# Kernel tuning notes

Measured on AMD Instinct MI355X. Metric: run time of the kernel, lower is better.

## Reference

```python
import jax, jax.numpy as jnp
import numpy as np

M = 8192      # number of simplices (edges)
F_IN = 32
F_OUT = 32
K1 = 3        # lower Laplacian filter order
K2 = 3        # upper Laplacian filter order


def setup_inputs() -> dict:
    key = jax.random.key(0)
    kx, kl, ku, kw = jax.random.split(key, 4)
    x = jax.random.normal(kx, (M, F_IN), dtype=jnp.float32)
    # scale Laplacians so the Chebyshev recursion stays numerically tame
    scale = 1.0 / np.sqrt(M)
    Ll = jax.random.normal(kl, (M, M), dtype=jnp.float32) * scale
    Lu = jax.random.normal(ku, (M, M), dtype=jnp.float32) * scale
    # xavier-uniform-ish init for W (F_in, F_out, 1+K1+K2)
    gain = np.sqrt(2.0)  # relu gain as in reset_parameters
    bound = gain * np.sqrt(6.0 / (F_IN + F_OUT))
    W = jax.random.uniform(kw, (F_IN, F_OUT, 1 + K1 + K2), dtype=jnp.float32,
                           minval=-bound, maxval=bound)
    return {"x": x, "Ll": Ll, "Lu": Lu, "W": W}


def chebyshev(L, K, x):
    """Chebyshev terms T_1..T_K of L applied to x, stacked on a trailing dim.
    T_0 = x, T_1 = L x, T_k = 2 L T_{k-1} - T_{k-2}. Returns [M, F, K]."""
    t_prev = x
    t_cur = L @ x
    terms = [t_cur]
    for _ in range(K - 1):
        t_next = 2.0 * (L @ t_cur) - t_prev
        t_prev, t_cur = t_cur, t_next
        terms.append(t_cur)
    return jnp.stack(terms, axis=2)


def reference(x, Ll, Lu, W):
    # identity term I @ x == x  -> [M, F_in, 1]
    Ix = x[:, :, None]
    Xl = chebyshev(Ll, K1, x)          # [M, F_in, K1]
    Xu = chebyshev(Lu, K2, x)          # [M, F_in, K2]
    X = jnp.concatenate([Ix, Xl, Xu], axis=2)  # [M, F_in, 1+K1+K2]
    # per-order projection; dropout has p=0.0 so it is the identity
    y = jnp.einsum('nik,iok->no', X, W)        # [M, F_out]
    return y
```

## Files before the change

kernel.cpp:

```cpp
#include <hip/hip_runtime.h>
#include <hip/hip_bf16.h>
#include <stdint.h>

#define Mdim 8192
#define KSTEPS 256

typedef __attribute__((ext_vector_type(8))) short short8v;
typedef __attribute__((ext_vector_type(4))) float f32x4;
typedef __attribute__((ext_vector_type(2))) float f32x2;

static __device__ __forceinline__ short bf16c(float f) {
  __hip_bfloat16 h = __float2bfloat16(f);
  union { __hip_bfloat16 h; short s; } c; c.h = h;
  return c.s;
}

__global__ __launch_bounds__(256)
void repack_x(const float* __restrict__ x, short* __restrict__ Bp)
{
  int t = blockIdx.x * 256 + threadIdx.x;
  int l = t & 63, h = (t >> 6) & 1, ks = t >> 7;
  int col = h * 16 + (l & 15);
  int kbase = ks * 32 + ((l >> 4) << 3);
  short8v v;
#pragma unroll
  for (int j = 0; j < 8; ++j) v[j] = bf16c(x[(size_t)(kbase + j) * 32 + col]);
  reinterpret_cast<short8v*>(Bp)[t] = v;
}

__global__ __launch_bounds__(256)
void convert_t1(const float* __restrict__ src, const short* __restrict__ Bx,
                short* __restrict__ dst, float* __restrict__ Pt1)
{
  __shared__ __align__(16) char sh[16 * 1032 * 2];
  short (*Lb)[1032] = reinterpret_cast<short (*)[1032]>(sh);

  const int tile = blockIdx.x >> 3;
  const int slab = blockIdx.x & 7;
  const int t = threadIdx.x;
  const int lane = t & 63;
  const int wid  = t >> 6;

  for (int i = 0; i < 16; ++i) {
    const f32x4* p = reinterpret_cast<const f32x4*>(
        src + ((size_t)tile * 16 + i) * Mdim + slab * 1024) + t;
    f32x4 a = __builtin_nontemporal_load(p);
    short* q = &Lb[i][t * 4];
    q[0] = bf16c(a[0]); q[1] = bf16c(a[1]); q[2] = bf16c(a[2]); q[3] = bf16c(a[3]);
  }
  __syncthreads();

  const short8v* bx8 = reinterpret_cast<const short8v*>(Bx);
  f32x4 acc0 = {0.f, 0.f, 0.f, 0.f};
  f32x4 acc1 = {0.f, 0.f, 0.f, 0.f};
#pragma unroll
  for (int it = 0; it < 8; ++it) {
    const int ksl = it * 4 + wid;
    short8v av = *reinterpret_cast<const short8v*>(
        &Lb[lane & 15][ksl * 32 + ((lane >> 4) << 3)]);
    reinterpret_cast<short8v*>(dst)[(size_t)(tile * 256 + slab * 32 + ksl) * 64 + lane] = av;
    const int gks = slab * 32 + ksl;
    short8v b0 = bx8[(size_t)(gks << 1) * 64 + lane];
    short8v b1 = bx8[(size_t)((gks << 1) + 1) * 64 + lane];
    acc0 = __builtin_amdgcn_mfma_f32_16x16x32_bf16(av, b0, acc0, 0, 0, 0);
    acc1 = __builtin_amdgcn_mfma_f32_16x16x32_bf16(av, b1, acc1, 0, 0, 0);
  }

  __syncthreads();
  float* Clf = reinterpret_cast<float*>(sh);
  {
    const int crow = (lane >> 4) << 2;
    const int ccol = lane & 15;
#pragma unroll
    for (int q = 0; q < 4; ++q) {
      Clf[((wid * 16) + crow + q) * 32 + ccol] = acc0[q];
      Clf[((wid * 16) + crow + q) * 32 + 16 + ccol] = acc1[q];
    }
  }
  __syncthreads();
  {
    const int e = t * 2;
    const int row = e >> 5, col = e & 31;
    float v0 = Clf[row * 32 + col] + Clf[(16 + row) * 32 + col]
             + Clf[(32 + row) * 32 + col] + Clf[(48 + row) * 32 + col];
    float v1 = Clf[row * 32 + col + 1] + Clf[(16 + row) * 32 + col + 1]
             + Clf[(32 + row) * 32 + col + 1] + Clf[(48 + row) * 32 + col + 1];
    f32x2 o; o[0] = v0; o[1] = v1;
    *reinterpret_cast<f32x2*>(Pt1 + (size_t)(tile * 8 + slab) * 512 + e) = o;
  }
}

__global__ __launch_bounds__(256)
void reduce_t1(const float* __restrict__ Pt1, float* __restrict__ Tout,
               short* __restrict__ BpOut)
{
  __shared__ float Cred[16][32];
  const int tile = blockIdx.x;
  const int t = threadIdx.x;
  const int e = t * 2;
  float s0 = 0.f, s1 = 0.f;
#pragma unroll
  for (int s = 0; s < 8; ++s) {
    f32x2 v = *reinterpret_cast<const f32x2*>(Pt1 + (size_t)(tile * 8 + s) * 512 + e);
    s0 += v[0]; s1 += v[1];
  }
  f32x2 o; o[0] = s0; o[1] = s1;
  *reinterpret_cast<f32x2*>(Tout + (size_t)tile * 512 + e) = o;
  Cred[e >> 5][e & 31] = s0;
  Cred[e >> 5][(e & 31) + 1] = s1;
  __syncthreads();
  if (t < 64) {
    const int r0 = tile << 4;
    const int ksOut = r0 >> 5;
    const int sub = (r0 >> 4) & 1;
    const int h = t >> 5;
    const int lp = (t & 31) + sub * 32;
    const int col = h * 16 + (lp & 15);
    const int lrbase = (lp & 16) ? 8 : 0;
    short8v v;
#pragma unroll
    for (int j = 0; j < 8; ++j) v[j] = bf16c(Cred[lrbase + j][col]);
    reinterpret_cast<short8v*>(BpOut)[(ksOut << 1 | h) * 64 + lp] = v;
  }
}

template<int HASPREV>
__global__ __launch_bounds__(512)
void gemm_stage(const short* __restrict__ As, const short* __restrict__ Bps,
                const float* __restrict__ Tprev, float* __restrict__ Tout,
                short* __restrict__ BpOut)
{
  const int bTile = blockIdx.x;
  const int lane = threadIdx.x & 63;
  const int wid  = threadIdx.x >> 6;
  const int r0 = bTile << 4;
  const int ksbase = wid * 32;

  const short8v* aF = reinterpret_cast<const short8v*>(As)
                      + ((size_t)bTile * 256 + ksbase) * 64 + lane;
  const short8v* bF = reinterpret_cast<const short8v*>(Bps)
                      + (size_t)ksbase * 128 + lane;

  f32x4 acc0 = {0.f, 0.f, 0.f, 0.f};
  f32x4 acc1 = {0.f, 0.f, 0.f, 0.f};

#pragma unroll 8
  for (int ks = 0; ks < 32; ++ks) {
    short8v av = aF[ks * 64];
    short8v b0 = bF[ks * 128];
    short8v b1 = bF[ks * 128 + 64];
    acc0 = __builtin_amdgcn_mfma_f32_16x16x32_bf16(av, b0, acc0, 0, 0, 0);
    acc1 = __builtin_amdgcn_mfma_f32_16x16x32_bf16(av, b1, acc1, 0, 0, 0);
  }

  __shared__ float Cl[8][16][32];
  __shared__ float Cred[16][32];
  {
    const int crow = (lane >> 4) << 2;
    const int ccol = lane & 15;
#pragma unroll
    for (int q = 0; q < 4; ++q) {
      Cl[wid][crow + q][ccol] = acc0[q];
      Cl[wid][crow + q][16 + ccol] = acc1[q];
    }
  }
  __syncthreads();
  {
    const int t = threadIdx.x;
    const int row = t >> 5, col = t & 31;
    float v = Cl[0][row][col] + Cl[1][row][col] + Cl[2][row][col] + Cl[3][row][col]
            + Cl[4][row][col] + Cl[5][row][col] + Cl[6][row][col] + Cl[7][row][col];
    if constexpr (HASPREV) {
      v = 2.f * v - Tprev[(size_t)r0 * 32 + t];
    }
    Tout[(size_t)r0 * 32 + t] = v;
    Cred[row][col] = v;
  }
  __syncthreads();
  if (threadIdx.x < 64) {
    const int t = threadIdx.x;
    const int ksOut = r0 >> 5;
    const int sub = (r0 >> 4) & 1;
    const int h = t >> 5;
    const int lp = (t & 31) + sub * 32;
    const int col = h * 16 + (lp & 15);
    const int lrbase = (lp & 16) ? 8 : 0;
    short8v v;
#pragma unroll
    for (int j = 0; j < 8; ++j) v[j] = bf16c(Cred[lrbase + j][col]);
    reinterpret_cast<short8v*>(BpOut)[(ksOut << 1 | h) * 64 + lp] = v;
  }
}

template<int HASPREV>
__global__ __launch_bounds__(512)
void gemm_f32_stage(const float* __restrict__ Af, const short8v* __restrict__ Bp,
                    const float* __restrict__ Tprev, float* __restrict__ Tout,
                    short* __restrict__ BpOut)
{
  const int lane = threadIdx.x & 63;
  const int wid  = threadIdx.x >> 6;
  const int r0 = blockIdx.x << 4;
  const int arow = r0 + (lane & 15);
  const int koff = (lane >> 4) << 3;
  const int ksbase = wid * 32;

  f32x4 acc0 = {0.f, 0.f, 0.f, 0.f};
  f32x4 acc1 = {0.f, 0.f, 0.f, 0.f};

  const float* ap = Af + (size_t)arow * Mdim + ksbase * 32 + koff;
#pragma unroll 8
  for (int ks = 0; ks < 32; ++ks) {
    const int g = ksbase + ks;
    f32x4 a0 = *reinterpret_cast<const f32x4*>(ap);
    f32x4 a1 = *reinterpret_cast<const f32x4*>(ap + 4);
    short8v av;
#pragma unroll
    for (int j = 0; j < 4; ++j) av[j] = bf16c(a0[j]);
#pragma unroll
    for (int j = 0; j < 4; ++j) av[4 + j] = bf16c(a1[j]);
    short8v b0 = Bp[(g << 1) * 64 + lane];
    short8v b1 = Bp[((g << 1) + 1) * 64 + lane];
    acc0 = __builtin_amdgcn_mfma_f32_16x16x32_bf16(av, b0, acc0, 0, 0, 0);
    acc1 = __builtin_amdgcn_mfma_f32_16x16x32_bf16(av, b1, acc1, 0, 0, 0);
    ap += 32;
  }

  __shared__ float Cl[8][16][32];
  __shared__ float Cred[16][32];
  {
    const int crow = (lane >> 4) << 2;
    const int ccol = lane & 15;
#pragma unroll
    for (int q = 0; q < 4; ++q) {
      Cl[wid][crow + q][ccol] = acc0[q];
      Cl[wid][crow + q][16 + ccol] = acc1[q];
    }
  }
  __syncthreads();
  {
    const int t = threadIdx.x;
    const int row = t >> 5, col = t & 31;
    float v = Cl[0][row][col] + Cl[1][row][col] + Cl[2][row][col] + Cl[3][row][col]
            + Cl[4][row][col] + Cl[5][row][col] + Cl[6][row][col] + Cl[7][row][col];
    if constexpr (HASPREV) {
      v = 2.f * v - Tprev[(size_t)r0 * 32 + t];
    }
    Tout[(size_t)r0 * 32 + t] = v;
    Cred[row][col] = v;
  }
  __syncthreads();
  if (threadIdx.x < 64) {
    const int t = threadIdx.x;
    const int ksOut = r0 >> 5;
    const int sub = (r0 >> 4) & 1;
    const int h = t >> 5;
    const int lp = (t & 31) + sub * 32;
    const int col = h * 16 + (lp & 15);
    const int lrbase = (lp & 16) ? 8 : 0;
    short8v v;
#pragma unroll
    for (int j = 0; j < 8; ++j) v[j] = bf16c(Cred[lrbase + j][col]);
    reinterpret_cast<short8v*>(BpOut)[(ksOut << 1 | h) * 64 + lp] = v;
  }
}

__global__ __launch_bounds__(256)
void combine(const float* __restrict__ x,
             const float* __restrict__ T1l, const float* __restrict__ T2l,
             const float* __restrict__ T3l, const float* __restrict__ T1u,
             const float* __restrict__ T2u, const float* __restrict__ T3u,
             const float* __restrict__ W, float* __restrict__ y)
{
  __shared__ float Wl[7168];
  for (int i = threadIdx.x; i < 7168; i += 256) Wl[i] = W[i];
  __syncthreads();
  int t = blockIdx.x * 256 + threadIdx.x;
  int n = t >> 5, o = t & 31;
  const float* Xs[7] = {x, T1l, T2l, T3l, T1u, T2u, T3u};
  float sum = 0.f;
#pragma unroll
  for (int k = 0; k < 7; ++k) {
    const f32x4* Xr = reinterpret_cast<const f32x4*>(Xs[k] + (size_t)n * 32);
#pragma unroll
    for (int i4 = 0; i4 < 8; ++i4) {
      f32x4 xv = Xr[i4];
#pragma unroll
      for (int j = 0; j < 4; ++j)
        sum += xv[j] * Wl[(i4 * 4 + j) * 224 + o * 7 + k];
    }
  }
  y[t] = sum;
}

extern "C" void kernel_launch(void* const* d_in, const int* in_sizes, int n_in,
                              void* d_out, int out_size, void* d_ws, size_t ws_size,
                              hipStream_t stream)
{
  const float* x  = (const float*)d_in[0];
  const float* Ll = (const float*)d_in[1];
  const float* Lu = (const float*)d_in[2];
  const float* W  = (const float*)d_in[3];
  float* y = (float*)d_out;

  char* ws = (char*)d_ws;
  size_t off = 0;
  auto alloc = [&](size_t bytes) -> void* {
    void* p = ws + off; off += (bytes + 255) & ~(size_t)255; return p;
  };
  short* Bx = (short*)alloc(512 * 1024);
  short* B1 = (short*)alloc(512 * 1024);
  short* B2 = (short*)alloc(512 * 1024);
  float* T1l = (float*)alloc(1u << 20);
  float* T2l = (float*)alloc(1u << 20);
  float* T3l = (float*)alloc(1u << 20);
  float* T1u = (float*)alloc(1u << 20);
  float* T2u = (float*)alloc(1u << 20);
  float* T3u = (float*)alloc(1u << 20);
  float* Pt1 = (float*)alloc((size_t)512 * 8 * 512 * 4);

  const size_t lbytes = (size_t)Mdim * Mdim * sizeof(short);
  bool useBF = (ws_size >= off + lbytes);
  short* Lab = nullptr;
  if (useBF) Lab = (short*)alloc(lbytes);

  repack_x<<<128, 256, 0, stream>>>(x, Bx);

  if (useBF) {
    convert_t1<<<4096, 256, 0, stream>>>(Ll, Bx, Lab, Pt1);
    reduce_t1<<<512, 256, 0, stream>>>(Pt1, T1l, B1);
    gemm_stage<1><<<512, 512, 0, stream>>>(Lab, B1, x,   T2l, B2);
    gemm_stage<1><<<512, 512, 0, stream>>>(Lab, B2, T1l, T3l, B1);
    convert_t1<<<4096, 256, 0, stream>>>(Lu, Bx, Lab, Pt1);
    reduce_t1<<<512, 256, 0, stream>>>(Pt1, T1u, B1);
    gemm_stage<1><<<512, 512, 0, stream>>>(Lab, B1, x,   T2u, B2);
    gemm_stage<1><<<512, 512, 0, stream>>>(Lab, B2, T1u, T3u, B1);
  } else {
    gemm_f32_stage<0><<<512,512,0,stream>>>(Ll, (const short8v*)Bx, nullptr, T1l, B1);
    gemm_f32_stage<1><<<512,512,0,stream>>>(Ll, (const short8v*)B1, x,      T2l, B2);
    gemm_f32_stage<1><<<512,512,0,stream>>>(Ll, (const short8v*)B2, T1l,    T3l, B1);
    gemm_f32_stage<0><<<512,512,0,stream>>>(Lu, (const short8v*)Bx, nullptr, T1u, B1);
    gemm_f32_stage<1><<<512,512,0,stream>>>(Lu, (const short8v*)B1, x,      T2u, B2);
    gemm_f32_stage<1><<<512,512,0,stream>>>(Lu, (const short8v*)B2, T1u,    T3u, B1);
  }

  combine<<<1024, 256, 0, stream>>>(x, T1l, T2l, T3l, T1u, T2u, T3u, W, y);
}
```

Measured before the change: 253.2 us.

## Fuse last lower-Laplacian GEMM stage with upper-Laplacian conversion in one launch

The bf16 Laplacian buffer is split into two separate buffers, one for Ll and one for Lu. That lets the third Ll Chebyshev GEMM stage run in the same grid as the fp32-to-bf16 conversion of Lu, since the two kernels no longer share a workspace. Convert blocks grow to 512 threads, and the final stages skip the unused bf16 B-operand repack. This overlaps a compute-bound stage with a bandwidth-bound one and removes a launch. In exchange it needs twice the workspace, and it falls back to the fp32 path if that space is missing.

```diff
diff --git a/kernel.cpp b/kernel.cpp
--- a/kernel.cpp
+++ b/kernel.cpp
@@ -6,6 +6,7 @@
 #define KSTEPS 256
 
 typedef __attribute__((ext_vector_type(8))) short short8v;
+typedef __attribute__((ext_vector_type(4))) short short4v;
 typedef __attribute__((ext_vector_type(4))) float f32x4;
 typedef __attribute__((ext_vector_type(2))) float f32x2;
 
@@ -28,25 +29,26 @@
   reinterpret_cast<short8v*>(Bp)[t] = v;
 }
 
-__global__ __launch_bounds__(256)
-void convert_t1(const float* __restrict__ src, const short* __restrict__ Bx,
-                short* __restrict__ dst, float* __restrict__ Pt1)
-{
-  __shared__ __align__(16) char sh[16 * 1032 * 2];
-  short (*Lb)[1032] = reinterpret_cast<short (*)[1032]>(sh);
-
-  const int tile = blockIdx.x >> 3;
-  const int slab = blockIdx.x & 7;
+static __device__ __forceinline__ void convert_body(
+    char* sh, const float* __restrict__ src, const short* __restrict__ Bx,
+    short* __restrict__ dst, float* __restrict__ Pt1, int job)
+{
+  short* Lb = reinterpret_cast<short*>(sh);
+  const int tile = job >> 3;
+  const int slab = job & 7;
   const int t = threadIdx.x;
   const int lane = t & 63;
   const int wid  = t >> 6;
 
-  for (int i = 0; i < 16; ++i) {
+#pragma unroll
+  for (int it = 0; it < 8; ++it) {
+    const int s = it * 512 + t;
+    const int r = s >> 8, c = s & 255;
     const f32x4* p = reinterpret_cast<const f32x4*>(
-        src + ((size_t)tile * 16 + i) * Mdim + slab * 1024) + t;
+        src + ((size_t)tile * 16 + r) * Mdim + slab * 1024) + c;
     f32x4 a = __builtin_nontemporal_load(p);
-    short* q = &Lb[i][t * 4];
-    q[0] = bf16c(a[0]); q[1] = bf16c(a[1]); q[2] = bf16c(a[2]); q[3] = bf16c(a[3]);
+    short4v v; v[0] = bf16c(a[0]); v[1] = bf16c(a[1]); v[2] = bf16c(a[2]); v[3] = bf16c(a[3]);
+    *reinterpret_cast<short4v*>(&Lb[r * 1032 + c * 4]) = v;
   }
   __syncthreads();
 
@@ -54,10 +56,10 @@
   f32x4 acc0 = {0.f, 0.f, 0.f, 0.f};
   f32x4 acc1 = {0.f, 0.f, 0.f, 0.f};
 #pragma unroll
-  for (int it = 0; it < 8; ++it) {
-    const int ksl = it * 4 + wid;
+  for (int it = 0; it < 4; ++it) {
+    const int ksl = it * 8 + wid;
     short8v av = *reinterpret_cast<const short8v*>(
-        &Lb[lane & 15][ksl * 32 + ((lane >> 4) << 3)]);
+        &Lb[(lane & 15) * 1032 + ksl * 32 + ((lane >> 4) << 3)]);
     reinterpret_cast<short8v*>(dst)[(size_t)(tile * 256 + slab * 32 + ksl) * 64 + lane] = av;
     const int gks = slab * 32 + ksl;
     short8v b0 = bx8[(size_t)(gks << 1) * 64 + lane];
@@ -79,58 +81,20 @@
   }
   __syncthreads();
   {
-    const int e = t * 2;
-    const int row = e >> 5, col = e & 31;
-    float v0 = Clf[row * 32 + col] + Clf[(16 + row) * 32 + col]
-             + Clf[(32 + row) * 32 + col] + Clf[(48 + row) * 32 + col];
-    float v1 = Clf[row * 32 + col + 1] + Clf[(16 + row) * 32 + col + 1]
-             + Clf[(32 + row) * 32 + col + 1] + Clf[(48 + row) * 32 + col + 1];
-    f32x2 o; o[0] = v0; o[1] = v1;
-    *reinterpret_cast<f32x2*>(Pt1 + (size_t)(tile * 8 + slab) * 512 + e) = o;
-  }
-}
-
-__global__ __launch_bounds__(256)
-void reduce_t1(const float* __restrict__ Pt1, float* __restrict__ Tout,
-               short* __restrict__ BpOut)
-{
-  __shared__ float Cred[16][32];
-  const int tile = blockIdx.x;
-  const int t = threadIdx.x;
-  const int e = t * 2;
-  float s0 = 0.f, s1 = 0.f;
-#pragma unroll
-  for (int s = 0; s < 8; ++s) {
-    f32x2 v = *reinterpret_cast<const f32x2*>(Pt1 + (size_t)(tile * 8 + s) * 512 + e);
-    s0 += v[0]; s1 += v[1];
-  }
-  f32x2 o; o[0] = s0; o[1] = s1;
-  *reinterpret_cast<f32x2*>(Tout + (size_t)tile * 512 + e) = o;
-  Cred[e >> 5][e & 31] = s0;
-  Cred[e >> 5][(e & 31) + 1] = s1;
-  __syncthreads();
-  if (t < 64) {
-    const int r0 = tile << 4;
-    const int ksOut = r0 >> 5;
-    const int sub = (r0 >> 4) & 1;
-    const int h = t >> 5;
-    const int lp = (t & 31) + sub * 32;
-    const int col = h * 16 + (lp & 15);
-    const int lrbase = (lp & 16) ? 8 : 0;
-    short8v v;
-#pragma unroll
-    for (int j = 0; j < 8; ++j) v[j] = bf16c(Cred[lrbase + j][col]);
-    reinterpret_cast<short8v*>(BpOut)[(ksOut << 1 | h) * 64 + lp] = v;
-  }
-}
-
-template<int HASPREV>
-__global__ __launch_bounds__(512)
-void gemm_stage(const short* __restrict__ As, const short* __restrict__ Bps,
-                const float* __restrict__ Tprev, float* __restrict__ Tout,
-                short* __restrict__ BpOut)
-{
-  const int bTile = blockIdx.x;
+    const int row = t >> 5, col = t & 31;
+    float v = 0.f;
+#pragma unroll
+    for (int s = 0; s < 8; ++s) v += Clf[((s * 16) + row) * 32 + col];
+    Pt1[(size_t)job * 512 + t] = v;
+  }
+}
+
+template<int WRITEB>
+static __device__ __forceinline__ void gemm_body(
+    char* sh, const short* __restrict__ As, const short* __restrict__ Bps,
+    const float* __restrict__ Tprev, float* __restrict__ Tout,
+    short* __restrict__ BpOut, int bTile)
+{
   const int lane = threadIdx.x & 63;
   const int wid  = threadIdx.x >> 6;
   const int r0 = bTile << 4;
@@ -153,32 +117,99 @@
     acc1 = __builtin_amdgcn_mfma_f32_16x16x32_bf16(av, b1, acc1, 0, 0, 0);
   }
 
-  __shared__ float Cl[8][16][32];
-  __shared__ float Cred[16][32];
+  float* Cl   = reinterpret_cast<float*>(sh);
+  float* Cred = reinterpret_cast<float*>(sh + 16384);
   {
     const int crow = (lane >> 4) << 2;
     const int ccol = lane & 15;
 #pragma unroll
     for (int q = 0; q < 4; ++q) {
-      Cl[wid][crow + q][ccol] = acc0[q];
-      Cl[wid][crow + q][16 + ccol] = acc1[q];
+      Cl[((wid * 16) + crow + q) * 32 + ccol] = acc0[q];
+      Cl[((wid * 16) + crow + q) * 32 + 16 + ccol] = acc1[q];
     }
   }
   __syncthreads();
   {
     const int t = threadIdx.x;
     const int row = t >> 5, col = t & 31;
-    float v = Cl[0][row][col] + Cl[1][row][col] + Cl[2][row][col] + Cl[3][row][col]
-            + Cl[4][row][col] + Cl[5][row][col] + Cl[6][row][col] + Cl[7][row][col];
-    if constexpr (HASPREV) {
-      v = 2.f * v - Tprev[(size_t)r0 * 32 + t];
-    }
+    float v = 0.f;
+#pragma unroll
+    for (int s = 0; s < 8; ++s) v += Cl[((s * 16) + row) * 32 + col];
+    v = 2.f * v - Tprev[(size_t)r0 * 32 + t];
     Tout[(size_t)r0 * 32 + t] = v;
-    Cred[row][col] = v;
-  }
-  __syncthreads();
-  if (threadIdx.x < 64) {
-    const int t = threadIdx.x;
+    if constexpr (WRITEB) Cred[row * 32 + col] = v;
+  }
+  if constexpr (WRITEB) {
+    __syncthreads();
+    if (threadIdx.x < 64) {
+      const int t = threadIdx.x;
+      const int ksOut = r0 >> 5;
+      const int sub = (r0 >> 4) & 1;
+      const int h = t >> 5;
+      const int lp = (t & 31) + sub * 32;
+      const int col = h * 16 + (lp & 15);
+      const int lrbase = (lp & 16) ? 8 : 0;
+      short8v v;
+#pragma unroll
+      for (int j = 0; j < 8; ++j) v[j] = bf16c(Cred[(lrbase + j) * 32 + col]);
+      reinterpret_cast<short8v*>(BpOut)[(ksOut << 1 | h) * 64 + lp] = v;
+    }
+  }
+}
+
+__global__ __launch_bounds__(512)
+void convert_t1(const float* __restrict__ src, const short* __restrict__ Bx,
+                short* __restrict__ dst, float* __restrict__ Pt1)
+{
+  __shared__ __align__(16) char sh[33024];
+  convert_body(sh, src, Bx, dst, Pt1, blockIdx.x);
+}
+
+template<int WRITEB>
+__global__ __launch_bounds__(512)
+void gemm_stage(const short* __restrict__ As, const short* __restrict__ Bps,
+                const float* __restrict__ Tprev, float* __restrict__ Tout,
+                short* __restrict__ BpOut)
+{
+  __shared__ __align__(16) char sh[18432];
+  gemm_body<WRITEB>(sh, As, Bps, Tprev, Tout, BpOut, blockIdx.x);
+}
+
+__global__ __launch_bounds__(512)
+void fused_conv_s3(const float* __restrict__ srcU, const short* __restrict__ Bx,
+                   short* __restrict__ dstU, float* __restrict__ Pt1u,
+                   const short* __restrict__ AsL, const short* __restrict__ BpsL,
+                   const float* __restrict__ TprevL, float* __restrict__ ToutL)
+{
+  __shared__ __align__(16) char sh[33024];
+  if (blockIdx.x < 512) {
+    gemm_body<0>(sh, AsL, BpsL, TprevL, ToutL, nullptr, blockIdx.x);
+  } else {
+    convert_body(sh, srcU, Bx, dstU, Pt1u, blockIdx.x - 512);
+  }
+}
+
+__global__ __launch_bounds__(256)
+void reduce_t1(const float* __restrict__ Pt1, float* __restrict__ Tout,
+               short* __restrict__ BpOut)
+{
+  __shared__ float Cred[16][32];
+  const int tile = blockIdx.x;
+  const int t = threadIdx.x;
+  const int e = t * 2;
+  float s0 = 0.f, s1 = 0.f;
+#pragma unroll
+  for (int s = 0; s < 8; ++s) {
+    f32x2 v = *reinterpret_cast<const f32x2*>(Pt1 + (size_t)(tile * 8 + s) * 512 + e);
+    s0 += v[0]; s1 += v[1];
+  }
+  f32x2 o; o[0] = s0; o[1] = s1;
+  *reinterpret_cast<f32x2*>(Tout + (size_t)tile * 512 + e) = o;
+  Cred[e >> 5][e & 31] = s0;
+  Cred[e >> 5][(e & 31) + 1] = s1;
+  __syncthreads();
+  if (t < 64) {
+    const int r0 = tile << 4;
     const int ksOut = r0 >> 5;
     const int sub = (r0 >> 4) & 1;
     const int h = t >> 5;
@@ -320,21 +351,21 @@
   float* Pt1 = (float*)alloc((size_t)512 * 8 * 512 * 4);
 
   const size_t lbytes = (size_t)Mdim * Mdim * sizeof(short);
-  bool useBF = (ws_size >= off + lbytes);
-  short* Lab = nullptr;
-  if (useBF) Lab = (short*)alloc(lbytes);
+  bool useBF = (ws_size >= off + 2 * lbytes);
+  short* Llb = nullptr; short* Lub = nullptr;
+  if (useBF) { Llb = (short*)alloc(lbytes); Lub = (short*)alloc(lbytes); }
 
   repack_x<<<128, 256, 0, stream>>>(x, Bx);
 
   if (useBF) {
-    convert_t1<<<4096, 256, 0, stream>>>(Ll, Bx, Lab, Pt1);
+    convert_t1<<<4096, 512, 0, stream>>>(Ll, Bx, Llb, Pt1);
     reduce_t1<<<512, 256, 0, stream>>>(Pt1, T1l, B1);
-    gemm_stage<1><<<512, 512, 0, stream>>>(Lab, B1, x,   T2l, B2);
-    gemm_stage<1><<<512, 512, 0, stream>>>(Lab, B2, T1l, T3l, B1);
-    convert_t1<<<4096, 256, 0, stream>>>(Lu, Bx, Lab, Pt1);
+    gemm_stage<1><<<512, 512, 0, stream>>>(Llb, B1, x, T2l, B2);
+    fused_conv_s3<<<4608, 512, 0, stream>>>(Lu, Bx, Lub, Pt1,
+                                            Llb, B2, T1l, T3l);
     reduce_t1<<<512, 256, 0, stream>>>(Pt1, T1u, B1);
-    gemm_stage<1><<<512, 512, 0, stream>>>(Lab, B1, x,   T2u, B2);
-    gemm_stage<1><<<512, 512, 0, stream>>>(Lab, B2, T1u, T3u, B1);
+    gemm_stage<1><<<512, 512, 0, stream>>>(Lub, B1, x, T2u, B2);
+    gemm_stage<0><<<512, 512, 0, stream>>>(Lub, B2, T1u, T3u, nullptr);
   } else {
     gemm_f32_stage<0><<<512,512,0,stream>>>(Ll, (const short8v*)Bx, nullptr, T1l, B1);
     gemm_f32_stage<1><<<512,512,0,stream>>>(Ll, (const short8v*)B1, x,      T2l, B2);
```

Result: slower. 267.8 us (+5.8%).
